# Kernel tuning notes

Hardware: AMD Instinct MI355X
Metric: run time of the kernel (lower is better)

Reference implementation:

```python
import jax, jax.numpy as jnp
import numpy as np
import math

D_MODEL = 256
N_HEADS = 4
D_HEAD = D_MODEL // N_HEADS  # 64
TT_RANK = 4
BATCH = 4
SEQ = 2048


def _xavier(key, shape):
    fan_in, fan_out = shape[0], shape[-1]
    if len(shape) == 4:  # (H, d, d, r) treated roughly like dense xavier
        fan_in, fan_out = shape[1], shape[2] * shape[3]
    lim = math.sqrt(6.0 / (fan_in + fan_out))
    return jax.random.uniform(key, shape, jnp.float32, -lim, lim)


def setup_inputs() -> dict:
    key = jax.random.key(0)
    ks = jax.random.split(key, 12)
    inp = {
        "query": jax.random.normal(ks[0], (BATCH, SEQ, D_MODEL), jnp.float32),
        "key": jax.random.normal(ks[1], (BATCH, SEQ, D_MODEL), jnp.float32),
        "value": jax.random.normal(ks[2], (BATCH, SEQ, D_MODEL), jnp.float32),
        "Wq": _xavier(ks[3], (D_MODEL, D_MODEL)),
        "bq": jnp.zeros((D_MODEL,), jnp.float32),
        "Wk": _xavier(ks[4], (D_MODEL, D_MODEL)),
        "bk": jnp.zeros((D_MODEL,), jnp.float32),
        "Wv": _xavier(ks[5], (D_MODEL, D_MODEL)),
        "bv": jnp.zeros((D_MODEL,), jnp.float32),
        "W2": _xavier(ks[6], (N_HEADS, D_HEAD, D_HEAD, TT_RANK)),
        "alpha": jnp.float32(0.5),  # nonzero so interaction path is exercised
        "Wo": _xavier(ks[7], (D_MODEL, D_MODEL)),
        "bo": jnp.zeros((D_MODEL,), jnp.float32),
    }
    return inp


def reference(query, key, value, Wq, bq, Wk, bk, Wv, bv, W2, alpha, Wo, bo):
    B, Sq, _ = query.shape
    Sk = key.shape[1]
    H, Dh = N_HEADS, D_HEAD

    # projections -> (B, H, S, Dh)
    Q = (query @ Wq + bq).reshape(B, Sq, H, Dh).transpose(0, 2, 1, 3)
    K = (key @ Wk + bk).reshape(B, Sk, H, Dh).transpose(0, 2, 1, 3)
    V = (value @ Wv + bv).reshape(B, Sk, H, Dh).transpose(0, 2, 1, 3)

    scale = math.sqrt(Dh)
    scores = jnp.einsum('bhqd,bhkd->bhqk', Q, K) / scale  # (B,H,Sq,Sk)

    # rank-2 tensor interaction: Qp[b,h,q,a,r] = sum_d Q[b,h,q,d] W2[h,d,a,r]
    #                            Kp[b,h,k,a,r] = sum_e K[b,h,k,e] W2[h,a,e,r]
    Qp = jnp.einsum('bhqd,hdar->bhqar', Q, W2)
    Kp = jnp.einsum('bhke,haer->bhkar', K, W2)
    interaction = jnp.einsum('bhqar,bhkar->bhqk', Qp, Kp) / (Dh * scale)

    total_scores = scores + alpha * interaction
    attn = jax.nn.softmax(total_scores, axis=-1)

    out = jnp.einsum('bhqk,bhkd->bhqd', attn, V)
    out = out.transpose(0, 2, 1, 3).reshape(B, Sq, H * Dh)
    return out @ Wo + bo
```

## Files before the change

kernel.cpp:

```cpp
#include <hip/hip_runtime.h>
#include <hip/hip_bf16.h>

#define BB   4
#define SS   2048
#define DM   256
#define HH   4
#define DHH  64
#define KSPL 2

typedef unsigned short ushort_t;
typedef unsigned int   uint_t;
using short8   = __attribute__((ext_vector_type(8))) short;
using ushort8  = __attribute__((ext_vector_type(8))) unsigned short;
using ushort4v = __attribute__((ext_vector_type(4))) unsigned short;
using float4v  = __attribute__((ext_vector_type(4))) float;

__device__ __forceinline__ ushort_t f2bf(float f) {
  uint_t u = __float_as_uint(f);
  uint_t r = (u + 0x7FFFu + ((u >> 16) & 1u)) >> 16;
  return (ushort_t)r;
}

__global__ __launch_bounds__(256) void k_pre(
    const float* __restrict__ Wk, const float* __restrict__ Wv,
    const float* __restrict__ Wo, const float* __restrict__ Wq,
    const float* __restrict__ bq, const float* __restrict__ W2,
    const float* __restrict__ alpha_p,
    ushort_t* __restrict__ WkT, ushort_t* __restrict__ WvT,
    ushort_t* __restrict__ WoT, ushort_t* __restrict__ WcT,
    float* __restrict__ bc) {
  __shared__ float sT[64 * 65];
  __shared__ __align__(16) float sM[64];
  const int t = threadIdx.x;
  const int bi = blockIdx.x;
  if (bi < 48) {
    int m = bi >> 4, tile = bi & 15;
    int ot = tile >> 2, ct = tile & 3;
    const float* src = (m == 0) ? Wk : (m == 1) ? Wv : Wo;
    ushort_t* dst = (m == 0) ? WkT : (m == 1) ? WvT : WoT;
#pragma unroll
    for (int it = 0; it < 16; ++it) {
      int i = it * 4 + (t >> 6), j = t & 63;
      sT[i * 65 + j] = src[(ct * 64 + i) * 256 + ot * 64 + j];
    }
    __syncthreads();
#pragma unroll
    for (int it = 0; it < 16; ++it) {
      int jj = it * 4 + (t >> 6), ii = t & 63;
      dst[(ot * 64 + jj) * 256 + ct * 64 + ii] = f2bf(sT[ii * 65 + jj]);
    }
  } else {
    int o = bi - 48;
    int h = o >> 6, e = o & 63;
    if (t < 64) {
      const float* Wd = W2 + h * 16384 + t * 256;
      const float* We = W2 + h * 16384 + e * 4;
      float s = 0.f;
#pragma unroll 8
      for (int a = 0; a < 64; ++a) {
        float4 x = *(const float4*)(Wd + a * 4);
        float4 y = *(const float4*)(We + a * 256);
        s += x.x * y.x + x.y * y.y + x.z * y.z + x.w * y.w;
      }
      sM[t] = (t == e ? 0.125f : 0.f) + alpha_p[0] * (1.f / 512.f) * s;
    }
    __syncthreads();
    const float* Wrow = Wq + t * 256 + h * 64;
    float s = 0.f;
#pragma unroll
    for (int d4 = 0; d4 < 16; ++d4) {
      float4 x = *(const float4*)(Wrow + d4 * 4);
      float4 mm = *(const float4*)(sM + d4 * 4);
      s += x.x * mm.x + x.y * mm.y + x.z * mm.z + x.w * mm.w;
    }
    WcT[o * 256 + t] = f2bf(s);
    if (t == 0) {
      float sb = 0.f;
      for (int d = 0; d < 64; ++d) sb += bq[h * 64 + d] * sM[d];
      bc[o] = sb;
    }
  }
}

template <int MODE>
__device__ __forceinline__ void pgemm(
    const ushort_t* __restrict__ sX, const ushort_t* __restrict__ WT,
    const float* __restrict__ bias, int w, int g, int l16,
    int b, int s0, ushort_t* __restrict__ dst) {
  float4v acc[2];
  acc[0] = (float4v){0.f, 0.f, 0.f, 0.f};
  acc[1] = (float4v){0.f, 0.f, 0.f, 0.f};
#pragma unroll
  for (int kc = 0; kc < 8; ++kc) {
    short8 af = *(const short8*)&sX[l16 * 256 + (((kc * 4 + g) ^ (l16 & 7)) << 3)];
#pragma unroll
    for (int ct = 0; ct < 2; ++ct) {
      int col = w * 32 + ct * 16 + l16;
      short8 bf = *(const short8*)&WT[col * 256 + kc * 32 + g * 8];
      acc[ct] = __builtin_amdgcn_mfma_f32_16x16x32_bf16(af, bf, acc[ct], 0, 0, 0);
    }
  }
#pragma unroll
  for (int ct = 0; ct < 2; ++ct) {
    int col = w * 32 + ct * 16 + l16;
    float bv = bias[col];
    int h = col >> 6, d = col & 63;
    if (MODE == 1) {
      ushort4v pk;
#pragma unroll
      for (int r = 0; r < 4; ++r) pk[r] = f2bf(acc[ct][r] + bv);
      *(ushort4v*)&dst[((size_t)(b * HH + h) * DHH + d) * SS + s0 + g * 4] = pk;
    } else {
#pragma unroll
      for (int r = 0; r < 4; ++r)
        dst[((size_t)(b * HH + h) * SS + s0 + g * 4 + r) * DHH + d] =
            f2bf(acc[ct][r] + bv);
    }
  }
}

__global__ __launch_bounds__(512) void k_proj(
    const float* __restrict__ q_in, const float* __restrict__ k_in,
    const float* __restrict__ v_in,
    const float* __restrict__ bk, const float* __restrict__ bv,
    const ushort_t* __restrict__ WcT, const ushort_t* __restrict__ WkT,
    const ushort_t* __restrict__ WvT, const float* __restrict__ bc,
    ushort_t* __restrict__ Qa, ushort_t* __restrict__ Ka,
    ushort_t* __restrict__ VTg) {
  __shared__ ushort_t sXq[16 * 256];
  __shared__ ushort_t sXk[16 * 256];
  __shared__ ushort_t sXv[16 * 256];

  const int t = threadIdx.x;
  const int w = t >> 6, lane = t & 63, g = lane >> 4, l16 = lane & 15;
  const int row0 = blockIdx.x * 16;
  const int b = row0 >> 11, s0 = row0 & (SS - 1);

  {
    int r = t >> 5, cf = (t & 31) * 8;
    int sw = r * 256 + (((cf >> 3) ^ (r & 7)) << 3);
    const float* qp = q_in + (size_t)(row0 + r) * DM + cf;
    const float* kp = k_in + (size_t)(row0 + r) * DM + cf;
    const float* vp = v_in + (size_t)(row0 + r) * DM + cf;
    float4 a0 = *(const float4*)qp, a1 = *(const float4*)(qp + 4);
    float4 b0 = *(const float4*)kp, b1 = *(const float4*)(kp + 4);
    float4 c0 = *(const float4*)vp, c1 = *(const float4*)(vp + 4);
    ushort8 uq, uk, uv;
    uq[0] = f2bf(a0.x); uq[1] = f2bf(a0.y); uq[2] = f2bf(a0.z); uq[3] = f2bf(a0.w);
    uq[4] = f2bf(a1.x); uq[5] = f2bf(a1.y); uq[6] = f2bf(a1.z); uq[7] = f2bf(a1.w);
    uk[0] = f2bf(b0.x); uk[1] = f2bf(b0.y); uk[2] = f2bf(b0.z); uk[3] = f2bf(b0.w);
    uk[4] = f2bf(b1.x); uk[5] = f2bf(b1.y); uk[6] = f2bf(b1.z); uk[7] = f2bf(b1.w);
    uv[0] = f2bf(c0.x); uv[1] = f2bf(c0.y); uv[2] = f2bf(c0.z); uv[3] = f2bf(c0.w);
    uv[4] = f2bf(c1.x); uv[5] = f2bf(c1.y); uv[6] = f2bf(c1.z); uv[7] = f2bf(c1.w);
    *(ushort8*)&sXq[sw] = uq;
    *(ushort8*)&sXk[sw] = uk;
    *(ushort8*)&sXv[sw] = uv;
  }
  __syncthreads();

  pgemm<0>(sXq, WcT, bc, w, g, l16, b, s0, Qa);
  pgemm<0>(sXk, WkT, bk, w, g, l16, b, s0, Ka);
  pgemm<1>(sXv, WvT, bv, w, g, l16, b, s0, VTg);
}

__global__ __launch_bounds__(256, 4) void k_attn(
    const ushort_t* __restrict__ Qa, const ushort_t* __restrict__ Ka,
    const ushort_t* __restrict__ VTg,
    float* __restrict__ Opart, float* __restrict__ lpart) {
  __shared__ ushort_t sKa[64 * 64];
  __shared__ ushort_t sVT[64 * 64];
  __shared__ ushort_t sPT[64 * 64];

  const int t = threadIdx.x;
  const int w = t >> 6, lane = t & 63, g = lane >> 4, l16 = lane & 15;
  const int bh = blockIdx.y;
  const int q0 = blockIdx.x * 64;
  const int ks = blockIdx.z;
  const int qrow = w * 16 + l16;

  short8 qfrag[2];
  {
    const ushort_t* qp = Qa + ((size_t)bh * SS + q0 + qrow) * DHH + g * 8;
    qfrag[0] = *(const short8*)(qp);
    qfrag[1] = *(const short8*)(qp + 32);
  }

  const ushort_t* KaB = Ka + (size_t)bh * SS * DHH + (size_t)ks * 1024 * DHH;
  const ushort_t* VTB = VTg + (size_t)bh * DHH * SS + ks * 1024;

  const int r0 = t >> 3, c0 = t & 7, r1 = r0 + 32;
  short8 pk0 = *(const short8*)(KaB + (size_t)r0 * DHH + c0 * 8);
  short8 pk1 = *(const short8*)(KaB + (size_t)r1 * DHH + c0 * 8);
  short8 pv0 = *(const short8*)(VTB + (size_t)r0 * SS + c0 * 8);
  short8 pv1 = *(const short8*)(VTB + (size_t)r1 * SS + c0 * 8);

  float l_run = 0.f;
  float4v oacc[4];
#pragma unroll
  for (int dj = 0; dj < 4; ++dj) oacc[dj] = (float4v){0.f, 0.f, 0.f, 0.f};

  const int sw0 = r0 * 64 + ((c0 ^ (r0 & 7)) << 3);
  const int sw1 = r1 * 64 + ((c0 ^ (r1 & 7)) << 3);

  for (int kch = 0; kch < 1024 / 64; ++kch) {
    __syncthreads();
    *(short8*)(sKa + sw0) = pk0;
    *(short8*)(sKa + sw1) = pk1;
    *(short8*)(sVT + sw0) = pv0;
    *(short8*)(sVT + sw1) = pv1;
    if (kch + 1 < 1024 / 64) {
      const ushort_t* kp = KaB + (size_t)(kch + 1) * 64 * DHH;
      pk0 = *(const short8*)(kp + (size_t)r0 * DHH + c0 * 8);
      pk1 = *(const short8*)(kp + (size_t)r1 * DHH + c0 * 8);
      pv0 = *(const short8*)(VTB + (size_t)r0 * SS + (kch + 1) * 64 + c0 * 8);
      pv1 = *(const short8*)(VTB + (size_t)r1 * SS + (kch + 1) * 64 + c0 * 8);
    }
    __syncthreads();

    float4v sacc[4];
#pragma unroll
    for (int kj = 0; kj < 4; ++kj)
      sacc[kj] = (float4v){-20.f, -20.f, -20.f, -20.f};
#pragma unroll
    for (int kc = 0; kc < 2; ++kc) {
#pragma unroll
      for (int kj = 0; kj < 4; ++kj) {
        int krow = kj * 16 + l16;
        short8 kf = *(const short8*)(sKa + krow * 64 +
                                     (((kc * 4 + g) ^ (krow & 7)) << 3));
        sacc[kj] = __builtin_amdgcn_mfma_f32_16x16x32_bf16(kf, qfrag[kc],
                                                           sacc[kj], 0, 0, 0);
      }
    }

    float lp = 0.f;
#pragma unroll
    for (int kj = 0; kj < 4; ++kj) {
      float p0 = __expf(sacc[kj][0]);
      float p1 = __expf(sacc[kj][1]);
      float p2 = __expf(sacc[kj][2]);
      float p3 = __expf(sacc[kj][3]);
      uint_t u01 = __builtin_amdgcn_perm(__float_as_uint(p1),
                                         __float_as_uint(p0), 0x07060302u);
      uint_t u23 = __builtin_amdgcn_perm(__float_as_uint(p3),
                                         __float_as_uint(p2), 0x07060302u);
      lp += __uint_as_float(__float_as_uint(p0) & 0xFFFF0000u);
      lp += __uint_as_float(__float_as_uint(p1) & 0xFFFF0000u);
      lp += __uint_as_float(__float_as_uint(p2) & 0xFFFF0000u);
      lp += __uint_as_float(__float_as_uint(p3) & 0xFFFF0000u);
      int kbase = kj * 16 + g * 4;
      uint2 pack; pack.x = u01; pack.y = u23;
      *(uint2*)(sPT + qrow * 64 + (((kbase >> 3) ^ (qrow & 7)) << 3) +
                (kbase & 7)) = pack;
    }
    l_run += lp;

#pragma unroll
    for (int ck = 0; ck < 2; ++ck) {
      short8 pa = *(const short8*)(sPT + qrow * 64 +
                                   (((ck * 4 + g) ^ (qrow & 7)) << 3));
#pragma unroll
      for (int dj = 0; dj < 4; ++dj) {
        int vrow = dj * 16 + l16;
        short8 vb = *(const short8*)(sVT + vrow * 64 +
                                     (((ck * 4 + g) ^ (vrow & 7)) << 3));
        oacc[dj] = __builtin_amdgcn_mfma_f32_16x16x32_bf16(pa, vb, oacc[dj],
                                                           0, 0, 0);
      }
    }
  }

  l_run += __shfl_xor(l_run, 16, 64);
  l_run += __shfl_xor(l_run, 32, 64);
  const int b = bh >> 2, h = bh & 3;
  if (g == 0)
    lpart[(size_t)ks * (8192 * 4) + ((size_t)b * SS + q0 + w * 16 + l16) * 4 + h] = l_run;
  float* Ob = Opart + (size_t)ks * 8192 * 256;
#pragma unroll
  for (int r = 0; r < 4; ++r) {
    size_t row = (size_t)b * SS + q0 + w * 16 + g * 4 + r;
#pragma unroll
    for (int dj = 0; dj < 4; ++dj)
      Ob[row * DM + h * DHH + dj * 16 + l16] = oacc[dj][r];
  }
}

__global__ __launch_bounds__(512) void k_out(
    const float* __restrict__ Opart, const float* __restrict__ lpart,
    const ushort_t* __restrict__ WoT, const float* __restrict__ bo,
    float* __restrict__ Out) {
  __shared__ ushort_t sA[16 * 256];
  const int t = threadIdx.x;
  const int w = t >> 6, lane = t & 63, g = lane >> 4, l16 = lane & 15;
  const int row0 = blockIdx.x * 16;
  {
    int r = t >> 5, cf = (t & 31) * 8;
    size_t row = row0 + r;
    int h = cf >> 6;
    float l = lpart[row * 4 + h] + lpart[8192 * 4 + row * 4 + h];
    float linv = 1.0f / l;
    const float* o0 = Opart + row * DM + cf;
    const float* o1 = Opart + (size_t)8192 * 256 + row * DM + cf;
    float4 a0 = *(const float4*)o0, a1 = *(const float4*)(o0 + 4);
    float4 b0 = *(const float4*)o1, b1 = *(const float4*)(o1 + 4);
    ushort8 u;
    u[0] = f2bf((a0.x + b0.x) * linv); u[1] = f2bf((a0.y + b0.y) * linv);
    u[2] = f2bf((a0.z + b0.z) * linv); u[3] = f2bf((a0.w + b0.w) * linv);
    u[4] = f2bf((a1.x + b1.x) * linv); u[5] = f2bf((a1.y + b1.y) * linv);
    u[6] = f2bf((a1.z + b1.z) * linv); u[7] = f2bf((a1.w + b1.w) * linv);
    *(ushort8*)&sA[r * 256 + (((cf >> 3) ^ (r & 7)) << 3)] = u;
  }
  __syncthreads();

  float4v acc[2];
  acc[0] = (float4v){0.f, 0.f, 0.f, 0.f};
  acc[1] = (float4v){0.f, 0.f, 0.f, 0.f};
#pragma unroll
  for (int kc = 0; kc < 8; ++kc) {
    short8 af = *(const short8*)&sA[l16 * 256 + (((kc * 4 + g) ^ (l16 & 7)) << 3)];
#pragma unroll
    for (int ct = 0; ct < 2; ++ct) {
      int col = w * 32 + ct * 16 + l16;
      short8 bf = *(const short8*)&WoT[col * 256 + kc * 32 + g * 8];
      acc[ct] = __builtin_amdgcn_mfma_f32_16x16x32_bf16(af, bf, acc[ct], 0, 0, 0);
    }
  }
#pragma unroll
  for (int ct = 0; ct < 2; ++ct) {
    int col = w * 32 + ct * 16 + l16;
    float bv = bo[col];
#pragma unroll
    for (int r = 0; r < 4; ++r)
      Out[(size_t)(row0 + g * 4 + r) * DM + col] = acc[ct][r] + bv;
  }
}

extern "C" void kernel_launch(void* const* d_in, const int* in_sizes, int n_in,
                              void* d_out, int out_size, void* d_ws, size_t ws_size,
                              hipStream_t stream) {
  (void)in_sizes; (void)n_in; (void)out_size; (void)ws_size;
  const float* q_in  = (const float*)d_in[0];
  const float* k_in  = (const float*)d_in[1];
  const float* v_in  = (const float*)d_in[2];
  const float* Wq    = (const float*)d_in[3];
  const float* bq    = (const float*)d_in[4];
  const float* Wk    = (const float*)d_in[5];
  const float* bk    = (const float*)d_in[6];
  const float* Wv    = (const float*)d_in[7];
  const float* bv    = (const float*)d_in[8];
  const float* W2    = (const float*)d_in[9];
  const float* alpha = (const float*)d_in[10];
  const float* Wo    = (const float*)d_in[11];
  const float* bo    = (const float*)d_in[12];
  float* out = (float*)d_out;

  char* ws = (char*)d_ws;
  ushort_t* Qa    = (ushort_t*)ws;
  ushort_t* Ka    = (ushort_t*)(ws + 4194304);
  ushort_t* VTg   = (ushort_t*)(ws + 8388608);
  float*    Opart = (float*)(ws + 12582912);
  float*    lpart = (float*)(ws + 29360128);
  ushort_t* WkT   = (ushort_t*)(ws + 29622272);
  ushort_t* WvT   = (ushort_t*)(ws + 29753344);
  ushort_t* WoT   = (ushort_t*)(ws + 29884416);
  ushort_t* WcT   = (ushort_t*)(ws + 30015488);
  float*    bc    = (float*)(ws + 30146560);

  hipLaunchKernelGGL(k_pre, dim3(304), dim3(256), 0, stream,
                     Wk, Wv, Wo, Wq, bq, W2, alpha, WkT, WvT, WoT, WcT, bc);
  hipLaunchKernelGGL(k_proj, dim3(512), dim3(512), 0, stream,
                     q_in, k_in, v_in, bk, bv, WcT, WkT, WvT, bc, Qa, Ka, VTg);
  hipLaunchKernelGGL(k_attn, dim3(32, 16, KSPL), dim3(256), 0, stream,
                     Qa, Ka, VTg, Opart, lpart);
  hipLaunchKernelGGL(k_out, dim3(512), dim3(512), 0, stream,
                     Opart, lpart, WoT, bo, out);
}
```

Measured before the change: 165.5 us.

## Process 128 query rows per attention block and split keys four ways

Each attention block now handles two 64-row query sub-tiles, so every K/V tile staged in shared memory feeds twice as many MFMAs. The key dimension is split four ways instead of two to keep the grid size the same, and k_out now sums four partials. The register prefetch of the next K/V tile is removed: loads happen synchronously right before the barrier. This exposes global-load latency, doubles partial-output traffic, and raises register and LDS use.

```diff
diff --git a/kernel.cpp b/kernel.cpp
--- a/kernel.cpp
+++ b/kernel.cpp
@@ -6,7 +6,8 @@
 #define DM   256
 #define HH   4
 #define DHH  64
-#define KSPL 2
+#define KSPL 4
+#define KLEN (SS / KSPL)
 
 typedef unsigned short ushort_t;
 typedef unsigned int   uint_t;
@@ -169,58 +170,57 @@
     float* __restrict__ Opart, float* __restrict__ lpart) {
   __shared__ ushort_t sKa[64 * 64];
   __shared__ ushort_t sVT[64 * 64];
-  __shared__ ushort_t sPT[64 * 64];
+  __shared__ ushort_t sPT[128 * 64];
 
   const int t = threadIdx.x;
   const int w = t >> 6, lane = t & 63, g = lane >> 4, l16 = lane & 15;
   const int bh = blockIdx.y;
-  const int q0 = blockIdx.x * 64;
+  const int q0 = blockIdx.x * 128;
   const int ks = blockIdx.z;
-  const int qrow = w * 16 + l16;
-
-  short8 qfrag[2];
-  {
-    const ushort_t* qp = Qa + ((size_t)bh * SS + q0 + qrow) * DHH + g * 8;
-    qfrag[0] = *(const short8*)(qp);
-    qfrag[1] = *(const short8*)(qp + 32);
-  }
-
-  const ushort_t* KaB = Ka + (size_t)bh * SS * DHH + (size_t)ks * 1024 * DHH;
-  const ushort_t* VTB = VTg + (size_t)bh * DHH * SS + ks * 1024;
+
+  short8 qfrag[2][2];
+#pragma unroll
+  for (int s = 0; s < 2; ++s) {
+    const ushort_t* qp =
+        Qa + ((size_t)bh * SS + q0 + s * 64 + w * 16 + l16) * DHH + g * 8;
+    qfrag[s][0] = *(const short8*)(qp);
+    qfrag[s][1] = *(const short8*)(qp + 32);
+  }
+
+  const ushort_t* KaB = Ka + (size_t)bh * SS * DHH + (size_t)ks * KLEN * DHH;
+  const ushort_t* VTB = VTg + (size_t)bh * DHH * SS + ks * KLEN;
 
   const int r0 = t >> 3, c0 = t & 7, r1 = r0 + 32;
-  short8 pk0 = *(const short8*)(KaB + (size_t)r0 * DHH + c0 * 8);
-  short8 pk1 = *(const short8*)(KaB + (size_t)r1 * DHH + c0 * 8);
-  short8 pv0 = *(const short8*)(VTB + (size_t)r0 * SS + c0 * 8);
-  short8 pv1 = *(const short8*)(VTB + (size_t)r1 * SS + c0 * 8);
-
-  float l_run = 0.f;
-  float4v oacc[4];
-#pragma unroll
-  for (int dj = 0; dj < 4; ++dj) oacc[dj] = (float4v){0.f, 0.f, 0.f, 0.f};
-
   const int sw0 = r0 * 64 + ((c0 ^ (r0 & 7)) << 3);
   const int sw1 = r1 * 64 + ((c0 ^ (r1 & 7)) << 3);
 
-  for (int kch = 0; kch < 1024 / 64; ++kch) {
+  float l_run[2] = {0.f, 0.f};
+  float4v oacc[2][4];
+#pragma unroll
+  for (int s = 0; s < 2; ++s)
+#pragma unroll
+    for (int dj = 0; dj < 4; ++dj) oacc[s][dj] = (float4v){0.f, 0.f, 0.f, 0.f};
+
+  for (int kch = 0; kch < KLEN / 64; ++kch) {
     __syncthreads();
-    *(short8*)(sKa + sw0) = pk0;
-    *(short8*)(sKa + sw1) = pk1;
-    *(short8*)(sVT + sw0) = pv0;
-    *(short8*)(sVT + sw1) = pv1;
-    if (kch + 1 < 1024 / 64) {
-      const ushort_t* kp = KaB + (size_t)(kch + 1) * 64 * DHH;
-      pk0 = *(const short8*)(kp + (size_t)r0 * DHH + c0 * 8);
-      pk1 = *(const short8*)(kp + (size_t)r1 * DHH + c0 * 8);
-      pv0 = *(const short8*)(VTB + (size_t)r0 * SS + (kch + 1) * 64 + c0 * 8);
-      pv1 = *(const short8*)(VTB + (size_t)r1 * SS + (kch + 1) * 64 + c0 * 8);
+    {
+      short8 k0 = *(const short8*)(KaB + (size_t)(kch * 64 + r0) * DHH + c0 * 8);
+      short8 k1 = *(const short8*)(KaB + (size_t)(kch * 64 + r1) * DHH + c0 * 8);
+      short8 v0 = *(const short8*)(VTB + (size_t)r0 * SS + kch * 64 + c0 * 8);
+      short8 v1 = *(const short8*)(VTB + (size_t)r1 * SS + kch * 64 + c0 * 8);
+      *(short8*)(sKa + sw0) = k0;
+      *(short8*)(sKa + sw1) = k1;
+      *(short8*)(sVT + sw0) = v0;
+      *(short8*)(sVT + sw1) = v1;
     }
     __syncthreads();
 
-    float4v sacc[4];
-#pragma unroll
-    for (int kj = 0; kj < 4; ++kj)
-      sacc[kj] = (float4v){-20.f, -20.f, -20.f, -20.f};
+    float4v sacc[2][4];
+#pragma unroll
+    for (int s = 0; s < 2; ++s)
+#pragma unroll
+      for (int kj = 0; kj < 4; ++kj)
+        sacc[s][kj] = (float4v){-20.f, -20.f, -20.f, -20.f};
 #pragma unroll
     for (int kc = 0; kc < 2; ++kc) {
 #pragma unroll
@@ -228,60 +228,77 @@
         int krow = kj * 16 + l16;
         short8 kf = *(const short8*)(sKa + krow * 64 +
                                      (((kc * 4 + g) ^ (krow & 7)) << 3));
-        sacc[kj] = __builtin_amdgcn_mfma_f32_16x16x32_bf16(kf, qfrag[kc],
-                                                           sacc[kj], 0, 0, 0);
+        sacc[0][kj] = __builtin_amdgcn_mfma_f32_16x16x32_bf16(
+            kf, qfrag[0][kc], sacc[0][kj], 0, 0, 0);
+        sacc[1][kj] = __builtin_amdgcn_mfma_f32_16x16x32_bf16(
+            kf, qfrag[1][kc], sacc[1][kj], 0, 0, 0);
       }
     }
 
-    float lp = 0.f;
-#pragma unroll
-    for (int kj = 0; kj < 4; ++kj) {
-      float p0 = __expf(sacc[kj][0]);
-      float p1 = __expf(sacc[kj][1]);
-      float p2 = __expf(sacc[kj][2]);
-      float p3 = __expf(sacc[kj][3]);
-      uint_t u01 = __builtin_amdgcn_perm(__float_as_uint(p1),
-                                         __float_as_uint(p0), 0x07060302u);
-      uint_t u23 = __builtin_amdgcn_perm(__float_as_uint(p3),
-                                         __float_as_uint(p2), 0x07060302u);
-      lp += __uint_as_float(__float_as_uint(p0) & 0xFFFF0000u);
-      lp += __uint_as_float(__float_as_uint(p1) & 0xFFFF0000u);
-      lp += __uint_as_float(__float_as_uint(p2) & 0xFFFF0000u);
-      lp += __uint_as_float(__float_as_uint(p3) & 0xFFFF0000u);
-      int kbase = kj * 16 + g * 4;
-      uint2 pack; pack.x = u01; pack.y = u23;
-      *(uint2*)(sPT + qrow * 64 + (((kbase >> 3) ^ (qrow & 7)) << 3) +
-                (kbase & 7)) = pack;
-    }
-    l_run += lp;
+#pragma unroll
+    for (int s = 0; s < 2; ++s) {
+      int qrow = s * 64 + w * 16 + l16;
+      float lp = 0.f;
+#pragma unroll
+      for (int kj = 0; kj < 4; ++kj) {
+        float p0 = __expf(sacc[s][kj][0]);
+        float p1 = __expf(sacc[s][kj][1]);
+        float p2 = __expf(sacc[s][kj][2]);
+        float p3 = __expf(sacc[s][kj][3]);
+        uint_t u01 = __builtin_amdgcn_perm(__float_as_uint(p1),
+                                           __float_as_uint(p0), 0x07060302u);
+        uint_t u23 = __builtin_amdgcn_perm(__float_as_uint(p3),
+                                           __float_as_uint(p2), 0x07060302u);
+        lp += __uint_as_float(__float_as_uint(p0) & 0xFFFF0000u);
+        lp += __uint_as_float(__float_as_uint(p1) & 0xFFFF0000u);
+        lp += __uint_as_float(__float_as_uint(p2) & 0xFFFF0000u);
+        lp += __uint_as_float(__float_as_uint(p3) & 0xFFFF0000u);
+        int kbase = kj * 16 + g * 4;
+        uint2 pack; pack.x = u01; pack.y = u23;
+        *(uint2*)(sPT + qrow * 64 + (((kbase >> 3) ^ (qrow & 7)) << 3) +
+                  (kbase & 7)) = pack;
+      }
+      l_run[s] += lp;
+    }
 
 #pragma unroll
     for (int ck = 0; ck < 2; ++ck) {
-      short8 pa = *(const short8*)(sPT + qrow * 64 +
-                                   (((ck * 4 + g) ^ (qrow & 7)) << 3));
+      short8 vb[4];
 #pragma unroll
       for (int dj = 0; dj < 4; ++dj) {
         int vrow = dj * 16 + l16;
-        short8 vb = *(const short8*)(sVT + vrow * 64 +
-                                     (((ck * 4 + g) ^ (vrow & 7)) << 3));
-        oacc[dj] = __builtin_amdgcn_mfma_f32_16x16x32_bf16(pa, vb, oacc[dj],
-                                                           0, 0, 0);
+        vb[dj] = *(const short8*)(sVT + vrow * 64 +
+                                  (((ck * 4 + g) ^ (vrow & 7)) << 3));
       }
-    }
-  }
-
-  l_run += __shfl_xor(l_run, 16, 64);
-  l_run += __shfl_xor(l_run, 32, 64);
+#pragma unroll
+      for (int s = 0; s < 2; ++s) {
+        int qrow = s * 64 + w * 16 + l16;
+        short8 pa = *(const short8*)(sPT + qrow * 64 +
+                                     (((ck * 4 + g) ^ (qrow & 7)) << 3));
+#pragma unroll
+        for (int dj = 0; dj < 4; ++dj)
+          oacc[s][dj] = __builtin_amdgcn_mfma_f32_16x16x32_bf16(
+              pa, vb[dj], oacc[s][dj], 0, 0, 0);
+      }
+    }
+  }
+
   const int b = bh >> 2, h = bh & 3;
-  if (g == 0)
-    lpart[(size_t)ks * (8192 * 4) + ((size_t)b * SS + q0 + w * 16 + l16) * 4 + h] = l_run;
-  float* Ob = Opart + (size_t)ks * 8192 * 256;
-#pragma unroll
-  for (int r = 0; r < 4; ++r) {
-    size_t row = (size_t)b * SS + q0 + w * 16 + g * 4 + r;
-#pragma unroll
-    for (int dj = 0; dj < 4; ++dj)
-      Ob[row * DM + h * DHH + dj * 16 + l16] = oacc[dj][r];
+  float* Ob = Opart + (size_t)ks * (8192 * 256);
+#pragma unroll
+  for (int s = 0; s < 2; ++s) {
+    l_run[s] += __shfl_xor(l_run[s], 16, 64);
+    l_run[s] += __shfl_xor(l_run[s], 32, 64);
+    if (g == 0)
+      lpart[(size_t)ks * (8192 * 4) +
+            ((size_t)b * SS + q0 + s * 64 + w * 16 + l16) * 4 + h] = l_run[s];
+#pragma unroll
+    for (int r = 0; r < 4; ++r) {
+      size_t row = (size_t)b * SS + q0 + s * 64 + w * 16 + g * 4 + r;
+#pragma unroll
+      for (int dj = 0; dj < 4; ++dj)
+        Ob[row * DM + h * DHH + dj * 16 + l16] = oacc[s][dj][r];
+    }
   }
 }
 
@@ -297,17 +314,23 @@
     int r = t >> 5, cf = (t & 31) * 8;
     size_t row = row0 + r;
     int h = cf >> 6;
-    float l = lpart[row * 4 + h] + lpart[8192 * 4 + row * 4 + h];
+    float l = 0.f;
+    float s0 = 0.f, s1 = 0.f, s2 = 0.f, s3 = 0.f,
+          s4 = 0.f, s5 = 0.f, s6 = 0.f, s7 = 0.f;
+#pragma unroll
+    for (int ks = 0; ks < KSPL; ++ks) {
+      l += lpart[(size_t)ks * (8192 * 4) + row * 4 + h];
+      const float* o = Opart + (size_t)ks * (8192 * 256) + row * DM + cf;
+      float4 a0 = *(const float4*)o, a1 = *(const float4*)(o + 4);
+      s0 += a0.x; s1 += a0.y; s2 += a0.z; s3 += a0.w;
+      s4 += a1.x; s5 += a1.y; s6 += a1.z; s7 += a1.w;
+    }
     float linv = 1.0f / l;
-    const float* o0 = Opart + row * DM + cf;
-    const float* o1 = Opart + (size_t)8192 * 256 + row * DM + cf;
-    float4 a0 = *(const float4*)o0, a1 = *(const float4*)(o0 + 4);
-    float4 b0 = *(const float4*)o1, b1 = *(const float4*)(o1 + 4);
     ushort8 u;
-    u[0] = f2bf((a0.x + b0.x) * linv); u[1] = f2bf((a0.y + b0.y) * linv);
-    u[2] = f2bf((a0.z + b0.z) * linv); u[3] = f2bf((a0.w + b0.w) * linv);
-    u[4] = f2bf((a1.x + b1.x) * linv); u[5] = f2bf((a1.y + b1.y) * linv);
-    u[6] = f2bf((a1.z + b1.z) * linv); u[7] = f2bf((a1.w + b1.w) * linv);
+    u[0] = f2bf(s0 * linv); u[1] = f2bf(s1 * linv);
+    u[2] = f2bf(s2 * linv); u[3] = f2bf(s3 * linv);
+    u[4] = f2bf(s4 * linv); u[5] = f2bf(s5 * linv);
+    u[6] = f2bf(s6 * linv); u[7] = f2bf(s7 * linv);
     *(ushort8*)&sA[r * 256 + (((cf >> 3) ^ (r & 7)) << 3)] = u;
   }
   __syncthreads();
@@ -359,19 +382,19 @@
   ushort_t* Ka    = (ushort_t*)(ws + 4194304);
   ushort_t* VTg   = (ushort_t*)(ws + 8388608);
   float*    Opart = (float*)(ws + 12582912);
-  float*    lpart = (float*)(ws + 29360128);
-  ushort_t* WkT   = (ushort_t*)(ws + 29622272);
-  ushort_t* WvT   = (ushort_t*)(ws + 29753344);
-  ushort_t* WoT   = (ushort_t*)(ws + 29884416);
-  ushort_t* WcT   = (ushort_t*)(ws + 30015488);
-  float*    bc    = (float*)(ws + 30146560);
+  float*    lpart = (float*)(ws + 46137344);
+  ushort_t* WkT   = (ushort_t*)(ws + 48234496);
+  ushort_t* WvT   = (ushort_t*)(ws + 48365568);
+  ushort_t* WoT   = (ushort_t*)(ws + 48496640);
+  ushort_t* WcT   = (ushort_t*)(ws + 48627712);
+  float*    bc    = (float*)(ws + 48758784);
 
   hipLaunchKernelGGL(k_pre, dim3(304), dim3(256), 0, stream,
                      Wk, Wv, Wo, Wq, bq, W2, alpha, WkT, WvT, WoT, WcT, bc);
   hipLaunchKernelGGL(k_proj, dim3(512), dim3(512), 0, stream,
                      q_in, k_in, v_in, bk, bv, WcT, WkT, WvT, bc, Qa, Ka, VTg);
-  hipLaunchKernelGGL(k_attn, dim3(32, 16, KSPL), dim3(256), 0, stream,
-                     Qa, Ka, VTg, Opart, lpart);
+  hipLaunchKernelGGL(k_attn, dim3(SS / 128, BB * HH, KSPL), dim3(256), 0,
+                     stream, Qa, Ka, VTg, Opart, lpart);
   hipLaunchKernelGGL(k_out, dim3(512), dim3(512), 0, stream,
                      Opart, lpart, WoT, bo, out);
 }
```

Result: no change. 164.1 us (-0.9%).
